# Optimization experiments

Measured on AMD Instinct MI355X. Metric: run time of the kernel, lower is better.

The kernel has to match this reference:

```python
import jax, jax.numpy as jnp
import numpy as np

B, S, D, H = 2, 2048, 1024, 16


def setup_inputs() -> dict:
    key = jax.random.key(0)
    ks = jax.random.split(key, 8)
    wscale = 1.0 / np.sqrt(D)  # ~xavier for square matrices
    return {
        "q": jax.random.normal(ks[0], (B, S, D), jnp.float32),
        "k": jax.random.normal(ks[1], (B, S, D), jnp.float32),
        "v": jax.random.normal(ks[2], (B, S, D), jnp.float32),
        "mask": jnp.tril(jnp.ones((S, S), jnp.int32))[None, None, :, :],  # [1,1,S,S] causal
        "Wq": jax.random.normal(ks[3], (D, D), jnp.float32) * wscale,
        "bq": jnp.zeros((D,), jnp.float32),
        "Wk": jax.random.normal(ks[4], (D, D), jnp.float32) * wscale,
        "bk": jnp.zeros((D,), jnp.float32),
        "Wv": jax.random.normal(ks[5], (D, D), jnp.float32) * wscale,
        "bv": jnp.zeros((D,), jnp.float32),
        "Wo": jax.random.normal(ks[6], (D, D), jnp.float32) * wscale,
        "bo": jnp.zeros((D,), jnp.float32),
    }


def reference(q, k, v, mask, Wq, bq, Wk, bk, Wv, bv, Wo, bo):
    batch_size, seq_len = q.shape[0], q.shape[1]
    qp = q @ Wq + bq
    kp = k @ Wk + bk
    vp = v @ Wv + bv
    qkv = jnp.concatenate([qp, kp, vp], axis=2)          # [B,S,3D]
    qkv = jnp.reshape(qkv, (batch_size, seq_len, H, -1), order='F')  # faithful Fortran-order head split
    qkv = qkv.transpose(0, 2, 1, 3)                      # [B,H,S,3*hd]
    qh, kh, vh = jnp.array_split(qkv, 3, axis=-1)        # each [B,H,S,hd]
    scores = qh @ jnp.swapaxes(kh, -2, -1) / kh.shape[-1] ** 0.5  # [B,H,S,S]
    scores = jnp.where(mask == 0, -9e15, scores)
    attention = jax.nn.softmax(scores, axis=-1)
    values = attention @ vh                              # [B,H,S,hd]
    values = values.transpose(0, 2, 1, 3).reshape(batch_size, seq_len, D)
    out = values @ Wo + bo
    return (out, attention)
```

## Files before the change

kernel.cpp:

```cpp
#include <hip/hip_runtime.h>
#include <stdint.h>

#define B_ 2
#define S_ 2048
#define D_ 1024
#define H_ 16
#define HD_ 64
#define BS_ 4096

typedef __bf16 bf16_t;
typedef __attribute__((ext_vector_type(8))) __bf16 bf16x8;
typedef __attribute__((ext_vector_type(4))) float f32x4;

#define VMCNT0 asm volatile("s_waitcnt vmcnt(0)" ::: "memory")
#define LGKMCNT0 asm volatile("s_waitcnt lgkmcnt(0)" ::: "memory")

__device__ __forceinline__ void barrier_raw() {
  asm volatile("" ::: "memory");
  __builtin_amdgcn_s_barrier();
  asm volatile("" ::: "memory");
}

__device__ __forceinline__ bf16_t f2bf(float f) {
  union { float f; uint32_t u; } v; v.f = f;
  uint32_t r = v.u + 0x7FFFu + ((v.u >> 16) & 1u);
  union { uint16_t u; bf16_t b; } o; o.u = (uint16_t)(r >> 16);
  return o.b;
}

__device__ __forceinline__ void gload_lds16(const void* g, void* l) {
  __builtin_amdgcn_global_load_lds((const __attribute__((address_space(1))) void*)g,
                                   (__attribute__((address_space(3))) void*)l,
                                   16, 0, 0);
}

__device__ __forceinline__ void stage64(const bf16_t* __restrict__ g, int gstride,
                                        bf16_t* lds, int wave, int lane) {
  #pragma unroll
  for (int i = 0; i < 2; ++i) {
    int lin = (wave * 2 + i) * 64 + lane;
    int row = lin >> 3, c = lin & 7;
    gload_lds16(g + (size_t)row * gstride + ((c ^ (row & 7)) << 3), (char*)lds + lin * 16);
  }
}

__device__ __forceinline__ void stage128(const bf16_t* __restrict__ g, int gstride,
                                         bf16_t* lds, int wave, int lane) {
  #pragma unroll
  for (int i = 0; i < 4; ++i) {
    int lin = (wave * 4 + i) * 64 + lane;
    int row = lin >> 3, c = lin & 7;
    gload_lds16(g + (size_t)row * gstride + ((c ^ (row & 7)) << 3), (char*)lds + lin * 16);
  }
}

__device__ __forceinline__ bf16x8 frag64(const bf16_t* lds, int row, int chunk) {
  return *(const bf16x8*)((const char*)lds + row * 128 + ((chunk ^ (row & 7)) << 4));
}

__global__ __launch_bounds__(256) void to_bf16_3_kernel(const float* __restrict__ q,
                                                        const float* __restrict__ k,
                                                        const float* __restrict__ v,
                                                        bf16_t* __restrict__ qb,
                                                        bf16_t* __restrict__ kb,
                                                        bf16_t* __restrict__ vb) {
  const int which = blockIdx.y;
  const float* in = which == 0 ? q : which == 1 ? k : v;
  bf16_t* out = which == 0 ? qb : which == 1 ? kb : vb;
  int i = (blockIdx.x * 256 + threadIdx.x) * 8;
  const float4* p = (const float4*)(in + i);
  float4 a = p[0], b = p[1];
  bf16x8 o;
  o[0] = f2bf(a.x); o[1] = f2bf(a.y); o[2] = f2bf(a.z); o[3] = f2bf(a.w);
  o[4] = f2bf(b.x); o[5] = f2bf(b.y); o[6] = f2bf(b.z); o[7] = f2bf(b.w);
  *(bf16x8*)(out + i) = o;
}

__global__ __launch_bounds__(256) void conv_weight4_kernel(const float* __restrict__ Wq,
                                                           const float* __restrict__ Wk,
                                                           const float* __restrict__ Wv,
                                                           const float* __restrict__ Wo,
                                                           bf16_t* __restrict__ wt_base) {
  const int which = blockIdx.z;
  const float* w = which == 0 ? Wq : which == 1 ? Wk : which == 2 ? Wv : Wo;
  bf16_t* wt = wt_base + (size_t)which * D_ * D_;
  const int permute = (which < 3) ? 1 : 0;
  const float scale = (which == 0) ? 0.125f : 1.0f;

  __shared__ float tile[64][65];
  int d0 = blockIdx.x * 64, o0 = blockIdx.y * 64;
  #pragma unroll
  for (int it = 0; it < 16; ++it) {
    int e = it * 256 + threadIdx.x;
    int r = e >> 6, c = e & 63;
    tile[r][c] = w[(size_t)(d0 + r) * D_ + o0 + c];
  }
  __syncthreads();
  #pragma unroll
  for (int it = 0; it < 16; ++it) {
    int e = it * 256 + threadIdx.x;
    int dd = e & 63, oo = e >> 6;
    int o = o0 + oo;
    int np = permute ? ((o & 15) * 64 + (o >> 4)) : o;
    wt[(size_t)np * D_ + d0 + dd] = f2bf(tile[dd][oo] * scale);
  }
}

__global__ __launch_bounds__(256) void perm_bias_kernel(const float* __restrict__ bq,
                                                        const float* __restrict__ bk,
                                                        const float* __restrict__ bv,
                                                        float* __restrict__ out) {
  int i = blockIdx.x * 256 + threadIdx.x;
  if (i >= 3 * D_) return;
  int which = i >> 10, n = i & 1023;
  int src = (n >> 6) + ((n & 63) << 4);
  const float* b = which == 0 ? bq : (which == 1 ? bk : bv);
  out[i] = b[src] * (which == 0 ? 0.125f : 1.0f);
}

__global__ __launch_bounds__(256) void gemm_qkv_kernel(const bf16_t* __restrict__ Aq,
                                                       const bf16_t* __restrict__ Ak,
                                                       const bf16_t* __restrict__ Av,
                                                       const bf16_t* __restrict__ Bt,
                                                       const float* __restrict__ bias,
                                                       bf16_t* __restrict__ Oq,
                                                       bf16_t* __restrict__ Ok,
                                                       bf16_t* __restrict__ Ov) {
  __shared__ bf16_t As[128 * 64];
  __shared__ bf16_t Bs[128 * 64];
  const int tid = threadIdx.x, wave = tid >> 6, lane = tid & 63;
  const int wm = wave >> 1, wn = wave & 1;
  const int lrow = lane & 15, kgrp = lane >> 4;
  const int row0 = blockIdx.x * 128;
  const int which = blockIdx.y >> 3;
  const int col0 = (blockIdx.y & 7) * 128;
  const bf16_t* A = which == 0 ? Aq : which == 1 ? Ak : Av;
  bf16_t* O = which == 0 ? Oq : which == 1 ? Ok : Ov;
  const bf16_t* Brow = Bt + (size_t)(which * 1024 + col0) * 1024;
  const float* bs = bias + which * 1024 + col0;

  f32x4 acc[4][4];
  #pragma unroll
  for (int i = 0; i < 4; ++i)
    #pragma unroll
    for (int j = 0; j < 4; ++j) acc[i][j] = (f32x4){0.f, 0.f, 0.f, 0.f};

  for (int k0 = 0; k0 < 1024; k0 += 64) {
    __syncthreads();
    stage128(A + (size_t)row0 * 1024 + k0, 1024, As, wave, lane);
    stage128(Brow + k0, 1024, Bs, wave, lane);
    VMCNT0;
    __syncthreads();
    #pragma unroll
    for (int kk = 0; kk < 2; ++kk) {
      bf16x8 af[4], bfv[4];
      #pragma unroll
      for (int mi = 0; mi < 4; ++mi) af[mi] = frag64(As, wm * 64 + mi * 16 + lrow, kk * 4 + kgrp);
      #pragma unroll
      for (int nj = 0; nj < 4; ++nj) bfv[nj] = frag64(Bs, wn * 64 + nj * 16 + lrow, kk * 4 + kgrp);
      #pragma unroll
      for (int mi = 0; mi < 4; ++mi)
        #pragma unroll
        for (int nj = 0; nj < 4; ++nj)
          acc[mi][nj] = __builtin_amdgcn_mfma_f32_16x16x32_bf16(af[mi], bfv[nj], acc[mi][nj], 0, 0, 0);
    }
  }

  #pragma unroll
  for (int mi = 0; mi < 4; ++mi)
    #pragma unroll
    for (int nj = 0; nj < 4; ++nj) {
      const int col = wn * 64 + nj * 16 + lrow;
      const float bv = bs[col];
      #pragma unroll
      for (int r = 0; r < 4; ++r) {
        const int row = row0 + wm * 64 + mi * 16 + kgrp * 4 + r;
        O[(size_t)row * 1024 + col0 + col] = f2bf(acc[mi][nj][r] + bv);
      }
    }
}

__global__ __launch_bounds__(256) void gemm_out_kernel(const bf16_t* __restrict__ A,
                                                       const bf16_t* __restrict__ Bt,
                                                       const float* __restrict__ bias,
                                                       float* __restrict__ Cout) {
  __shared__ bf16_t As[128 * 64];
  __shared__ bf16_t Bs[64 * 64];
  const int tid = threadIdx.x, wave = tid >> 6, lane = tid & 63;
  const int wm = wave >> 1, wn = wave & 1;
  const int lrow = lane & 15, kgrp = lane >> 4;
  const int row0 = blockIdx.x * 128;
  const int col0 = blockIdx.y * 64;

  f32x4 acc[4][2];
  #pragma unroll
  for (int i = 0; i < 4; ++i)
    #pragma unroll
    for (int j = 0; j < 2; ++j) acc[i][j] = (f32x4){0.f, 0.f, 0.f, 0.f};

  for (int k0 = 0; k0 < 1024; k0 += 64) {
    __syncthreads();
    stage128(A + (size_t)row0 * 1024 + k0, 1024, As, wave, lane);
    stage64(Bt + (size_t)col0 * 1024 + k0, 1024, Bs, wave, lane);
    VMCNT0;
    __syncthreads();
    #pragma unroll
    for (int kk = 0; kk < 2; ++kk) {
      bf16x8 af[4], bfv[2];
      #pragma unroll
      for (int mi = 0; mi < 4; ++mi) af[mi] = frag64(As, wm * 64 + mi * 16 + lrow, kk * 4 + kgrp);
      #pragma unroll
      for (int nj = 0; nj < 2; ++nj) bfv[nj] = frag64(Bs, wn * 32 + nj * 16 + lrow, kk * 4 + kgrp);
      #pragma unroll
      for (int mi = 0; mi < 4; ++mi)
        #pragma unroll
        for (int nj = 0; nj < 2; ++nj)
          acc[mi][nj] = __builtin_amdgcn_mfma_f32_16x16x32_bf16(af[mi], bfv[nj], acc[mi][nj], 0, 0, 0);
    }
  }

  #pragma unroll
  for (int mi = 0; mi < 4; ++mi)
    #pragma unroll
    for (int nj = 0; nj < 2; ++nj) {
      const int col = col0 + wn * 32 + nj * 16 + lrow;
      const float bv = bias[col];
      #pragma unroll
      for (int r = 0; r < 4; ++r) {
        const int row = row0 + wm * 64 + mi * 16 + kgrp * 4 + r;
        Cout[(size_t)row * 1024 + col] = acc[mi][nj][r] + bv;
      }
    }
}

__global__ __launch_bounds__(256) void transpose_v_kernel(const bf16_t* __restrict__ Vp,
                                                          bf16_t* __restrict__ Vt) {
  __shared__ bf16_t t[64][80];
  const int st = blockIdx.x, bh = blockIdx.y;
  const int b = bh >> 4, h = bh & 15;
  const int tid = threadIdx.x;
  #pragma unroll
  for (int i = 0; i < 2; ++i) {
    int lin = i * 256 + tid;
    int r = lin >> 3, c = (lin & 7) * 8;
    bf16x8 v8 = *(const bf16x8*)(Vp + ((size_t)(b * S_ + st * 64 + r)) * D_ + h * HD_ + c);
    *(bf16x8*)&t[r][c] = v8;
  }
  __syncthreads();
  #pragma unroll
  for (int i = 0; i < 2; ++i) {
    int lin = i * 256 + tid;
    int f = lin >> 3, c = (lin & 7) * 8;
    bf16x8 o;
    #pragma unroll
    for (int e = 0; e < 8; ++e) o[e] = t[c + e][f];
    *(bf16x8*)(Vt + ((size_t)bh * HD_ + f) * S_ + st * 64 + c) = o;
  }
}

__global__ __launch_bounds__(256, 4) void attn_kernel(const bf16_t* __restrict__ Q,
                                                      const bf16_t* __restrict__ K,
                                                      const bf16_t* __restrict__ Vt,
                                                      float* __restrict__ attn_out,
                                                      bf16_t* __restrict__ values) {
  __shared__ bf16_t KsB[2][64 * 64];
  __shared__ bf16_t VtsB[2][64 * 64];
  __shared__ bf16_t Ps[4][16 * 64];

  const int tid = threadIdx.x;
  const int wave = tid >> 6, lane = tid & 63;
  const int lrow = lane & 15, kgrp = lane >> 4;
  const int bh = blockIdx.y, b = bh >> 4, h = bh & 15;
  const size_t base = (size_t)b * S_ * D_ + (size_t)h * HD_;
  const size_t vbase = (size_t)bh * HD_ * S_;
  const int qt = (31 - (int)blockIdx.x + bh) & 31;
  const int qr0 = qt * 64;
  bf16_t* psw = &Ps[wave][0];

  const bf16_t* qp = Q + base + (size_t)(qr0 + wave * 16 + lrow) * D_ + kgrp * 8;
  bf16x8 aq[2];
  aq[0] = *(const bf16x8*)qp;
  aq[1] = *(const bf16x8*)(qp + 32);

  stage64(K + base, D_, KsB[0], wave, lane);
  VMCNT0; barrier_raw();

  float psum[4] = {0.f, 0.f, 0.f, 0.f};
  for (int kj = 0; kj <= qt; ++kj) {
    if (kj < qt) stage64(K + base + (size_t)(kj + 1) * 64 * D_, D_, KsB[(kj + 1) & 1], wave, lane);
    const bf16_t* Kc = KsB[kj & 1];
    f32x4 s[4];
    #pragma unroll
    for (int nj = 0; nj < 4; ++nj) {
      s[nj] = (f32x4){0.f, 0.f, 0.f, 0.f};
      #pragma unroll
      for (int kk = 0; kk < 2; ++kk)
        s[nj] = __builtin_amdgcn_mfma_f32_16x16x32_bf16(
            aq[kk], frag64(Kc, nj * 16 + lrow, kk * 4 + kgrp), s[nj], 0, 0, 0);
    }
    if (kj == qt) {
      #pragma unroll
      for (int nj = 0; nj < 4; ++nj)
        #pragma unroll
        for (int r = 0; r < 4; ++r) {
          int lrq = wave * 16 + kgrp * 4 + r;
          int lck = nj * 16 + lrow;
          psum[r] += (lck > lrq) ? 0.f : __expf(s[nj][r]);
        }
    } else {
      #pragma unroll
      for (int nj = 0; nj < 4; ++nj)
        #pragma unroll
        for (int r = 0; r < 4; ++r) psum[r] += __expf(s[nj][r]);
    }
    VMCNT0; barrier_raw();
  }

  float rl[4];
  #pragma unroll
  for (int r = 0; r < 4; ++r) {
    float t = psum[r];
    #pragma unroll
    for (int off = 1; off < 16; off <<= 1) t += __shfl_xor(t, off);
    rl[r] = 1.0f / t;
  }

  f32x4 o[4];
  #pragma unroll
  for (int nj = 0; nj < 4; ++nj) o[nj] = (f32x4){0.f, 0.f, 0.f, 0.f};

  stage64(K + base, D_, KsB[0], wave, lane);
  stage64(Vt + vbase, S_, VtsB[0], wave, lane);
  VMCNT0; barrier_raw();

  const int srow = lane >> 3, scol = lane & 7;

  for (int kj = 0; kj <= qt; ++kj) {
    if (kj < qt) {
      stage64(K + base + (size_t)(kj + 1) * 64 * D_, D_, KsB[(kj + 1) & 1], wave, lane);
      stage64(Vt + vbase + (kj + 1) * 64, S_, VtsB[(kj + 1) & 1], wave, lane);
    }
    __builtin_amdgcn_sched_barrier(0);
    const bf16_t* Kc = KsB[kj & 1];
    const bf16_t* Vc = VtsB[kj & 1];
    f32x4 s[4];
    #pragma unroll
    for (int nj = 0; nj < 4; ++nj) {
      s[nj] = (f32x4){0.f, 0.f, 0.f, 0.f};
      #pragma unroll
      for (int kk = 0; kk < 2; ++kk)
        s[nj] = __builtin_amdgcn_mfma_f32_16x16x32_bf16(
            aq[kk], frag64(Kc, nj * 16 + lrow, kk * 4 + kgrp), s[nj], 0, 0, 0);
    }
    #pragma unroll
    for (int nj = 0; nj < 4; ++nj)
      #pragma unroll
      for (int r = 0; r < 4; ++r) {
        int lrq = wave * 16 + kgrp * 4 + r;
        int lck = nj * 16 + lrow;
        float p = __expf(s[nj][r]) * rl[r];
        if (kj == qt && lck > lrq) p = 0.f;
        int prow = kgrp * 4 + r, pcol = nj * 16 + lrow;
        *(bf16_t*)((char*)psw + prow * 128 + (((pcol >> 3) ^ (prow & 7)) << 4) + (pcol & 7) * 2) = f2bf(p);
      }
    LGKMCNT0;

    #pragma unroll
    for (int g = 0; g < 2; ++g) {
      const int pr = g * 8 + srow;
      float* grow = attn_out + ((size_t)bh * S_ + qr0 + wave * 16 + pr) * S_ + kj * 64;
      #pragma unroll
      for (int i = 0; i < 2; ++i) {
        const uint32_t* w2 = (const uint32_t*)((const char*)psw + pr * 128 +
                                               (((i * 4 + (scol >> 1)) ^ (pr & 7)) << 4) + (scol & 1) * 8);
        float4 f;
        f.x = __uint_as_float(w2[0] << 16);
        f.y = __uint_as_float(w2[0] & 0xffff0000u);
        f.z = __uint_as_float(w2[1] << 16);
        f.w = __uint_as_float(w2[1] & 0xffff0000u);
        *(float4*)(grow + i * 32 + scol * 4) = f;
      }
    }

    bf16x8 pa[2];
    #pragma unroll
    for (int kk = 0; kk < 2; ++kk)
      pa[kk] = *(const bf16x8*)((const char*)psw + lrow * 128 + (((kk * 4 + kgrp) ^ (lrow & 7)) << 4));
    #pragma unroll
    for (int nj = 0; nj < 4; ++nj)
      #pragma unroll
      for (int kk = 0; kk < 2; ++kk)
        o[nj] = __builtin_amdgcn_mfma_f32_16x16x32_bf16(
            pa[kk], frag64(Vc, nj * 16 + lrow, kk * 4 + kgrp), o[nj], 0, 0, 0);

    asm volatile("s_waitcnt vmcnt(4)" ::: "memory");
    barrier_raw();
  }

  {
    const int cstart = (qt + 1) * 64;
    if (cstart < S_) {
      int r = tid >> 2;
      float4 z = make_float4(0.f, 0.f, 0.f, 0.f);
      float* rowp = attn_out + ((size_t)bh * S_ + qr0 + r) * S_;
      for (int c = cstart + (tid & 3) * 4; c < S_; c += 16) *(float4*)(rowp + c) = z;
    }
  }

  #pragma unroll
  for (int nj = 0; nj < 4; ++nj)
    #pragma unroll
    for (int r = 0; r < 4; ++r) {
      int grow = qr0 + wave * 16 + kgrp * 4 + r;
      values[(size_t)(b * S_ + grow) * D_ + h * HD_ + nj * 16 + lrow] = f2bf(o[nj][r]);
    }
}

extern "C" void kernel_launch(void* const* d_in, const int* in_sizes, int n_in,
                              void* d_out, int out_size, void* d_ws, size_t ws_size,
                              hipStream_t stream) {
  const float* q  = (const float*)d_in[0];
  const float* k  = (const float*)d_in[1];
  const float* v  = (const float*)d_in[2];
  const float* Wq = (const float*)d_in[4];
  const float* bq = (const float*)d_in[5];
  const float* Wk = (const float*)d_in[6];
  const float* bk = (const float*)d_in[7];
  const float* Wv = (const float*)d_in[8];
  const float* bv = (const float*)d_in[9];
  const float* Wo = (const float*)d_in[10];
  const float* bo = (const float*)d_in[11];

  char* ws = (char*)d_ws;
  bf16_t* qb    = (bf16_t*)ws;
  bf16_t* kb    = qb + (size_t)BS_ * D_;
  bf16_t* vb    = kb + (size_t)BS_ * D_;
  bf16_t* Wqt   = vb + (size_t)BS_ * D_;
  bf16_t* Wkt   = Wqt + (size_t)D_ * D_;
  bf16_t* Wvt   = Wkt + (size_t)D_ * D_;
  bf16_t* Wot   = Wvt + (size_t)D_ * D_;
  float*  bias3 = (float*)(Wot + (size_t)D_ * D_);
  bf16_t* Qp    = (bf16_t*)(bias3 + 3 * D_);
  bf16_t* Kp    = Qp + (size_t)BS_ * D_;
  bf16_t* Vp    = Kp + (size_t)BS_ * D_;
  bf16_t* Vt    = qb;
  bf16_t* Val   = kb;

  to_bf16_3_kernel<<<dim3(2048, 3), 256, 0, stream>>>(q, k, v, qb, kb, vb);
  conv_weight4_kernel<<<dim3(16, 16, 4), 256, 0, stream>>>(Wq, Wk, Wv, Wo, Wqt);
  perm_bias_kernel<<<12, 256, 0, stream>>>(bq, bk, bv, bias3);

  gemm_qkv_kernel<<<dim3(32, 24), 256, 0, stream>>>(qb, kb, vb, Wqt, bias3, Qp, Kp, Vp);
  transpose_v_kernel<<<dim3(32, 32), 256, 0, stream>>>(Vp, Vt);

  float* attn_out = (float*)d_out + (size_t)BS_ * D_;
  attn_kernel<<<dim3(32, 32), 256, 0, stream>>>(Qp, Kp, Vt, attn_out, Val);

  gemm_out_kernel<<<dim3(32, 16), 256, 0, stream>>>(Val, Wot, bo, (float*)d_out);
}
```

Measured before the change: 300.3 us.

## Software-pipeline P·V and attention store one tile behind QK^T

Restructures the attention loop so each iteration runs QK^T for the current key tile while doing the P·V MFMAs and fp32 attention-row stores for the previous tile, with an epilogue for the last tile. V staging moves to the same iteration it is consumed one step later, and the mid-loop LDS wait is removed. The aim is to overlap global stores and the second matmul with the first matmul instead of running them serially. It also changes the vmcnt wait accounting, which could under-wait for the final V tile.

New measurement: 302.9 us. No clear change (+0.9%).

```diff
diff --git a/kernel.cpp b/kernel.cpp
--- a/kernel.cpp
+++ b/kernel.cpp
@@ -330,19 +330,34 @@
   for (int nj = 0; nj < 4; ++nj) o[nj] = (f32x4){0.f, 0.f, 0.f, 0.f};
 
   stage64(K + base, D_, KsB[0], wave, lane);
-  stage64(Vt + vbase, S_, VtsB[0], wave, lane);
   VMCNT0; barrier_raw();
 
   const int srow = lane >> 3, scol = lane & 7;
 
   for (int kj = 0; kj <= qt; ++kj) {
-    if (kj < qt) {
-      stage64(K + base + (size_t)(kj + 1) * 64 * D_, D_, KsB[(kj + 1) & 1], wave, lane);
-      stage64(Vt + vbase + (kj + 1) * 64, S_, VtsB[(kj + 1) & 1], wave, lane);
-    }
+    if (kj < qt) stage64(K + base + (size_t)(kj + 1) * 64 * D_, D_, KsB[(kj + 1) & 1], wave, lane);
+    stage64(Vt + vbase + kj * 64, S_, VtsB[kj & 1], wave, lane);
     __builtin_amdgcn_sched_barrier(0);
+
+    bf16x8 pa0_, pa1_;
+    uint32_t w2buf[8];
+    if (kj > 0) {
+      pa0_ = *(const bf16x8*)((const char*)psw + lrow * 128 + ((kgrp ^ (lrow & 7)) << 4));
+      pa1_ = *(const bf16x8*)((const char*)psw + lrow * 128 + (((4 + kgrp) ^ (lrow & 7)) << 4));
+      #pragma unroll
+      for (int g = 0; g < 2; ++g) {
+        const int pr = g * 8 + srow;
+        #pragma unroll
+        for (int i = 0; i < 2; ++i) {
+          const uint32_t* w2 = (const uint32_t*)((const char*)psw + pr * 128 +
+                                                 (((i * 4 + (scol >> 1)) ^ (pr & 7)) << 4) + (scol & 1) * 8);
+          w2buf[(g * 2 + i) * 2] = w2[0];
+          w2buf[(g * 2 + i) * 2 + 1] = w2[1];
+        }
+      }
+    }
+
     const bf16_t* Kc = KsB[kj & 1];
-    const bf16_t* Vc = VtsB[kj & 1];
     f32x4 s[4];
     #pragma unroll
     for (int nj = 0; nj < 4; ++nj) {
@@ -352,6 +367,31 @@
         s[nj] = __builtin_amdgcn_mfma_f32_16x16x32_bf16(
             aq[kk], frag64(Kc, nj * 16 + lrow, kk * 4 + kgrp), s[nj], 0, 0, 0);
     }
+
+    if (kj > 0) {
+      #pragma unroll
+      for (int g = 0; g < 2; ++g) {
+        const int pr = g * 8 + srow;
+        float* grow = attn_out + ((size_t)bh * S_ + qr0 + wave * 16 + pr) * S_ + (kj - 1) * 64;
+        #pragma unroll
+        for (int i = 0; i < 2; ++i) {
+          uint32_t a = w2buf[(g * 2 + i) * 2], b2 = w2buf[(g * 2 + i) * 2 + 1];
+          float4 f;
+          f.x = __uint_as_float(a << 16);
+          f.y = __uint_as_float(a & 0xffff0000u);
+          f.z = __uint_as_float(b2 << 16);
+          f.w = __uint_as_float(b2 & 0xffff0000u);
+          *(float4*)(grow + i * 32 + scol * 4) = f;
+        }
+      }
+      const bf16_t* Vc = VtsB[(kj - 1) & 1];
+      #pragma unroll
+      for (int nj = 0; nj < 4; ++nj) {
+        o[nj] = __builtin_amdgcn_mfma_f32_16x16x32_bf16(pa0_, frag64(Vc, nj * 16 + lrow, kgrp), o[nj], 0, 0, 0);
+        o[nj] = __builtin_amdgcn_mfma_f32_16x16x32_bf16(pa1_, frag64(Vc, nj * 16 + lrow, 4 + kgrp), o[nj], 0, 0, 0);
+      }
+    }
+
     #pragma unroll
     for (int nj = 0; nj < 4; ++nj)
       #pragma unroll
@@ -363,12 +403,18 @@
         int prow = kgrp * 4 + r, pcol = nj * 16 + lrow;
         *(bf16_t*)((char*)psw + prow * 128 + (((pcol >> 3) ^ (prow & 7)) << 4) + (pcol & 7) * 2) = f2bf(p);
       }
-    LGKMCNT0;
-
+
+    if (kj == 0) { VMCNT0; } else { asm volatile("s_waitcnt vmcnt(4)" ::: "memory"); }
+    barrier_raw();
+  }
+
+  {
+    bf16x8 pa0_ = *(const bf16x8*)((const char*)psw + lrow * 128 + ((kgrp ^ (lrow & 7)) << 4));
+    bf16x8 pa1_ = *(const bf16x8*)((const char*)psw + lrow * 128 + (((4 + kgrp) ^ (lrow & 7)) << 4));
     #pragma unroll
     for (int g = 0; g < 2; ++g) {
       const int pr = g * 8 + srow;
-      float* grow = attn_out + ((size_t)bh * S_ + qr0 + wave * 16 + pr) * S_ + kj * 64;
+      float* grow = attn_out + ((size_t)bh * S_ + qr0 + wave * 16 + pr) * S_ + qt * 64;
       #pragma unroll
       for (int i = 0; i < 2; ++i) {
         const uint32_t* w2 = (const uint32_t*)((const char*)psw + pr * 128 +
@@ -381,20 +427,12 @@
         *(float4*)(grow + i * 32 + scol * 4) = f;
       }
     }
-
-    bf16x8 pa[2];
-    #pragma unroll
-    for (int kk = 0; kk < 2; ++kk)
-      pa[kk] = *(const bf16x8*)((const char*)psw + lrow * 128 + (((kk * 4 + kgrp) ^ (lrow & 7)) << 4));
-    #pragma unroll
-    for (int nj = 0; nj < 4; ++nj)
-      #pragma unroll
-      for (int kk = 0; kk < 2; ++kk)
-        o[nj] = __builtin_amdgcn_mfma_f32_16x16x32_bf16(
-            pa[kk], frag64(Vc, nj * 16 + lrow, kk * 4 + kgrp), o[nj], 0, 0, 0);
-
-    asm volatile("s_waitcnt vmcnt(4)" ::: "memory");
-    barrier_raw();
+    const bf16_t* Vc = VtsB[qt & 1];
+    #pragma unroll
+    for (int nj = 0; nj < 4; ++nj) {
+      o[nj] = __builtin_amdgcn_mfma_f32_16x16x32_bf16(pa0_, frag64(Vc, nj * 16 + lrow, kgrp), o[nj], 0, 0, 0);
+      o[nj] = __builtin_amdgcn_mfma_f32_16x16x32_bf16(pa1_, frag64(Vc, nj * 16 + lrow, 4 + kgrp), o[nj], 0, 0, 0);
+    }
   }
 
   {
```
